# Kernel tuning notes

Measured on AMD Instinct MI355X. Metric: run time of the kernel, lower is better.

## Reference

```python
import jax, jax.numpy as jnp
import numpy as np

TEMPERATURE = 0.07
BASE_TEMPERATURE = 0.07
ANCHOR_NUM = 256   # total_classes after hard-anchor sampling
N_VIEW = 16
FEAT_DIM = 256
NUM_CLASSES = 19


def setup_inputs() -> dict:
    key = jax.random.key(0)
    k1, k2 = jax.random.split(key)
    feats = jax.random.normal(k1, (ANCHOR_NUM, N_VIEW, FEAT_DIM), dtype=jnp.float32)
    # projection-head outputs are L2-normalized in the upstream network
    feats = feats / jnp.linalg.norm(feats, axis=-1, keepdims=True)
    labels = jax.random.randint(k2, (ANCHOR_NUM,), 0, NUM_CLASSES, dtype=jnp.int32)
    return {"feats": feats, "labels": labels}


def reference(feats, labels) -> jnp.ndarray:
    # feats: [A, V, D] sampled anchors; labels: [A] class ids
    A, V, D = feats.shape
    N = A * V
    dt = feats.dtype
    # torch.cat(torch.unbind(feats_, dim=1), dim=0) -> view-major ordering
    contrast = feats.transpose(1, 0, 2).reshape(N, D)          # [N, D]
    lbl = jnp.tile(labels, V)                                   # [N]

    logits = jnp.matmul(contrast, contrast.T) / jnp.asarray(TEMPERATURE, dt)  # [N, N]
    logits = logits - jax.lax.stop_gradient(jnp.max(logits, axis=1, keepdims=True))

    pos_mask = (lbl[:, None] == lbl[None, :]).astype(dt)        # [N, N]
    neg_mask = 1.0 - pos_mask
    diag = jnp.arange(N)
    pos_mask = pos_mask.at[diag, diag].set(0.0)                 # drop self-contrast

    exp_logits = jnp.exp(logits)
    neg_sum = jnp.sum(exp_logits * neg_mask, axis=1, keepdims=True)  # [N, 1]
    log_prob = logits - jnp.log(exp_logits + neg_sum)
    mean_log_prob_pos = jnp.sum(pos_mask * log_prob, axis=1) / jnp.sum(pos_mask, axis=1)
    loss = -(TEMPERATURE / BASE_TEMPERATURE) * mean_log_prob_pos
    return jnp.mean(loss)
```

## Files before the change

### kernel.cpp

```cpp
#include <hip/hip_runtime.h>
#include <hip/hip_bf16.h>

#define D_DIM   256
#define N_TOT   4096
#define N_ANCH  256
#define NGRP    32
#define NBLK    528
#define NPART   64
#define K1  20.60992915555662f
#define LN2 0.6931471805599453f
#define MAXNP    48

typedef __attribute__((ext_vector_type(8))) short bf16x8;
typedef __attribute__((ext_vector_type(4))) float f32x4;

#define MFMA(a, b, c) __builtin_amdgcn_mfma_f32_16x16x32_bf16((a), (b), (c), 0, 0, 0)

__device__ __forceinline__ bf16x8 cvt8(const float4 a, const float4 b) {
    union { uint32_t w[4]; bf16x8 v; } u;
    asm("v_cvt_pk_bf16_f32 %0, %1, %2" : "=v"(u.w[0]) : "v"(a.x), "v"(a.y));
    asm("v_cvt_pk_bf16_f32 %0, %1, %2" : "=v"(u.w[1]) : "v"(a.z), "v"(a.w));
    asm("v_cvt_pk_bf16_f32 %0, %1, %2" : "=v"(u.w[2]) : "v"(b.x), "v"(b.y));
    asm("v_cvt_pk_bf16_f32 %0, %1, %2" : "=v"(u.w[3]) : "v"(b.z), "v"(b.w));
    return u.v;
}

__global__ void __launch_bounds__(256, 2) k_pass1(const float* __restrict__ feats,
                                                  const int* __restrict__ labels,
                                                  float* __restrict__ partAll,
                                                  float* __restrict__ posBuf,
                                                  float* __restrict__ out) {
    __shared__ __align__(16) char lds[65536];
    __shared__ int labS[N_ANCH];
    __shared__ int cntS[32];
    __shared__ int metaRank[16], metaToff[16];

    if (blockIdx.x == 0 && threadIdx.x == 0) out[0] = 0.f;

    int swzId = (blockIdx.x & 7) * 66 + (blockIdx.x >> 3);
    int rem = swzId, g = 0;
    while (rem >= NGRP - g) { rem -= NGRP - g; ++g; }
    const int s = g + rem;

    const int tid = threadIdx.x;
    const int lane = tid & 63, wid = tid >> 6;
    const int lrow = lane & 15, khalf = lane >> 4;
    const int wr = wid >> 1, wc = wid & 1;

    labS[tid] = labels[tid];
    if (tid < 32) cntS[tid] = 0;
    __syncthreads();
    atomicAdd(&cntS[labS[tid]], 1);

    const char* aSrcF = (const char*)(feats + (size_t)g * 128 * D_DIM);
    const char* bSrcF = (const char*)(feats + (size_t)s * 128 * D_DIM);

    uint32_t LgF[8], Lw[8];
#pragma unroll
    for (int o = 0; o < 8; ++o) {
        uint32_t L = (uint32_t)(tid * 16 + o * 4096);
        LgF[o] = (L >> 8) * 1024 + ((L & 255) << 1);
        Lw[o]  = L ^ (((L >> 8) & 7u) << 4);
    }

    auto stage = [&](int kc) {
        float4 fa[8][2], fb[8][2];
#pragma unroll
        for (int o = 0; o < 8; ++o) {
            const char* pa = aSrcF + LgF[o] + kc * 512;
            const char* pb = bSrcF + LgF[o] + kc * 512;
            fa[o][0] = *(const float4*)pa;  fa[o][1] = *(const float4*)(pa + 16);
            fb[o][0] = *(const float4*)pb;  fb[o][1] = *(const float4*)(pb + 16);
        }
#pragma unroll
        for (int o = 0; o < 8; ++o) {
            *(bf16x8*)(lds + Lw[o])         = cvt8(fa[o][0], fa[o][1]);
            *(bf16x8*)(lds + 32768 + Lw[o]) = cvt8(fb[o][0], fb[o][1]);
        }
    };

    f32x4 acc[4][4];
#pragma unroll
    for (int m = 0; m < 4; ++m)
#pragma unroll
        for (int n = 0; n < 4; ++n)
            acc[m][n] = (f32x4){0.f, 0.f, 0.f, 0.f};

    const uint32_t swz = (uint32_t)((lrow & 7) << 4);
    auto compute = [&]() {
#pragma unroll
        for (int ks = 0; ks < 4; ++ks) {
            bf16x8 af[4], bfr[4];
#pragma unroll
            for (int m = 0; m < 4; ++m) {
                uint32_t row = (uint32_t)(wr * 64 + m * 16 + lrow);
                af[m] = *(const bf16x8*)(lds + ((row * 256 + ks * 64 + khalf * 16) ^ swz));
            }
#pragma unroll
            for (int n = 0; n < 4; ++n) {
                uint32_t row = (uint32_t)(wc * 64 + n * 16 + lrow);
                bfr[n] = *(const bf16x8*)(lds + 32768 + ((row * 256 + ks * 64 + khalf * 16) ^ swz));
            }
#pragma unroll
            for (int m = 0; m < 4; ++m)
#pragma unroll
                for (int n = 0; n < 4; ++n)
                    acc[m][n] = MFMA(af[m], bfr[n], acc[m][n]);
        }
    };

    stage(0);
    __syncthreads();

    {
        int aIdx = tid >> 4, q = tid & 15;
        int aAnchor = (aIdx < 8) ? (g * 8 + aIdx) : (s * 8 + aIdx - 8);
        int la = labS[aAnchor];
        int rk = 0, tf = 0;
        for (int b = q; b < aAnchor; b += 16) {
            int lb = labS[b];
            rk += (lb == la);
            tf += cntS[lb];
        }
#pragma unroll
        for (int msk = 1; msk < 16; msk <<= 1) {
            rk += __shfl_xor(rk, msk, 64);
            tf += __shfl_xor(tf, msk, 64);
        }
        if (q == 0) { metaRank[aIdx] = rk; metaToff[aIdx] = tf; }
    }

    compute();
    __syncthreads();
    stage(1);
    __syncthreads();
    compute();
    __syncthreads();

    const int raBase = g * 8 + wr * 4, caBase = s * 8 + wc * 4;
    int labR[4], offR[4], rankR[4], labC[4], rankC[4], offC[4];
#pragma unroll
    for (int m = 0; m < 4; ++m) {
        labR[m]  = labS[raBase + m];
        offR[m]  = metaToff[wr * 4 + m];
        rankR[m] = metaRank[wr * 4 + m];
    }
#pragma unroll
    for (int n = 0; n < 4; ++n) {
        labC[n]  = labS[caBase + n];
        rankC[n] = metaRank[8 + wc * 4 + n];
        offC[n]  = metaToff[8 + wc * 4 + n];
    }

    float aAll[4][4];
    float colP[4];
#pragma unroll
    for (int m = 0; m < 4; ++m)
#pragma unroll
        for (int i = 0; i < 4; ++i) aAll[m][i] = 0.f;
#pragma unroll
    for (int n = 0; n < 4; ++n) colP[n] = 0.f;

    float* scr = (float*)lds + wid * 256;

#pragma unroll
    for (int m = 0; m < 4; ++m) {
#pragma unroll
        for (int n = 0; n < 4; ++n) {
            f32x4 c = acc[m][n];
            float e[4];
#pragma unroll
            for (int i = 0; i < 4; ++i) {
                e[i] = exp2f(__builtin_fmaf(c[i], K1, -K1));
                aAll[m][i] += e[i];
            }
            if (g != s)
                colP[n] += e[0] + e[1] + e[2] + e[3];
            if (labR[m] == labC[n]) {
                *(f32x4*)(posBuf + (size_t)(offR[m] + rankC[n]) * 256 + lane * 4) = c;
                if (g != s) {
#pragma unroll
                    for (int i = 0; i < 4; ++i)
                        scr[(khalf * 4 + i) * 16 + lrow] = c[i];
                    __builtin_amdgcn_s_waitcnt(0);
                    f32x4 tr = *(f32x4*)(scr + lrow * 16 + khalf * 4);
                    *(f32x4*)(posBuf + (size_t)(offC[n] + rankR[m]) * 256 + lane * 4) = tr;
                }
            }
        }
    }

#pragma unroll
    for (int msk = 1; msk < 16; msk <<= 1)
#pragma unroll
        for (int m = 0; m < 4; ++m)
#pragma unroll
            for (int i = 0; i < 4; ++i)
                aAll[m][i] += __shfl_xor(aAll[m][i], msk, 64);

    if (lrow == 0) {
#pragma unroll
        for (int m = 0; m < 4; ++m)
#pragma unroll
            for (int i = 0; i < 4; ++i) {
                int row = g * 128 + wr * 64 + m * 16 + khalf * 4 + i;
                partAll[row * NPART + s * 2 + wc] = aAll[m][i];
            }
    }

    if (g != s) {
#pragma unroll
        for (int msk = 16; msk < 64; msk <<= 1)
#pragma unroll
            for (int n = 0; n < 4; ++n)
                colP[n] += __shfl_xor(colP[n], msk, 64);
        if (lane < 16) {
#pragma unroll
            for (int n = 0; n < 4; ++n) {
                int row = s * 128 + wc * 64 + n * 16 + lane;
                partAll[row * NPART + g * 2 + wr] = colP[n];
            }
        }
    }
}

__global__ void __launch_bounds__(256) k_passB(const float* __restrict__ posBuf,
                                               const int* __restrict__ labels,
                                               const float* __restrict__ partAll,
                                               float* __restrict__ out) {
    int rt  = blockIdx.x;
    int tid = threadIdx.x;
    int l = tid >> 2, i = tid & 3;
    int r   = (l >> 4) * 4 + i;
    int col = l & 15;

    __shared__ float tile[MAXNP * 256];
    __shared__ float shA[16][17];
    __shared__ float shB[16][17];
    __shared__ float nsSh[16], PSh[16];
    __shared__ int labS[N_ANCH];
    __shared__ int cntS[32];
    __shared__ int wRk[4], wTf[4];
    __shared__ int mNp, mOff, mRank;

    labS[tid] = labels[tid];
    if (tid < 32) cntS[tid] = 0;
    __syncthreads();
    atomicAdd(&cntS[labS[tid]], 1);
    __syncthreads();
    {
        int la = labS[rt];
        int rk = 0, tf = 0;
        if (tid < rt) { int lb = labS[tid]; rk = (lb == la) ? 1 : 0; tf = cntS[lb]; }
#pragma unroll
        for (int msk = 1; msk < 64; msk <<= 1) {
            rk += __shfl_xor(rk, msk, 64);
            tf += __shfl_xor(tf, msk, 64);
        }
        if ((tid & 63) == 0) { wRk[tid >> 6] = rk; wTf[tid >> 6] = tf; }
        __syncthreads();
        if (tid == 0) {
            mNp   = cntS[la];
            mRank = wRk[0] + wRk[1] + wRk[2] + wRk[3];
            mOff  = wTf[0] + wTf[1] + wTf[2] + wTf[3];
        }
        __syncthreads();
    }
    int np = mNp, off = mOff, selfRank = mRank;

    float sE = 0.f, sP = 0.f;
    const float* src = posBuf + (size_t)off * 256 + tid;
    for (int j = 0; j < np; ++j) {
        float c = src[j * 256];
        tile[j * 256 + tid] = c;
        float l2 = __builtin_fmaf(c, K1, -K1);
        sE += exp2f(l2);
        bool diag = (j == selfRank) & (col == r);
        sP += diag ? 0.f : l2;
    }
    shA[r][col] = sE;
    shB[r][col] = sP;
    __syncthreads();
    if (tid < 16) {
        float e = 0.f, p = 0.f;
#pragma unroll
        for (int cc = 0; cc < 16; ++cc) { e += shA[tid][cc]; p += shB[tid][cc]; }
        const float* pa = partAll + (size_t)(rt * 16 + tid) * NPART;
        float sall = 0.f;
#pragma unroll
        for (int q = 0; q < 16; ++q) {
            float4 v = *(const float4*)(pa + q * 4);
            sall += v.x + v.y + v.z + v.w;
        }
        nsSh[tid] = sall - e;
        PSh[tid]  = p;
    }
    __syncthreads();

    float nsv = nsSh[r];
    float sL = 0.f;
    for (int j = 0; j < np; ++j) {
        float c  = tile[j * 256 + tid];
        float l2 = __builtin_fmaf(c, K1, -K1);
        float lg = __log2f(exp2f(l2) + nsv);
        bool diag = (j == selfRank) & (col == r);
        sL += diag ? 0.f : lg;
    }
    __syncthreads();
    shA[r][col] = sL;
    __syncthreads();
    if (tid < 16) {
        float L = 0.f;
#pragma unroll
        for (int cc = 0; cc < 16; ++cc) L += shA[tid][cc];
        float npRow = (float)(16 * np - 1);
        shB[0][tid] = (PSh[tid] - L) / npRow;
    }
    __syncthreads();
    if (tid == 0) {
        float sx = 0.f;
#pragma unroll
        for (int q = 0; q < 16; ++q) sx += shB[0][q];
        atomicAdd(out, -sx * (LN2 / (float)N_TOT));
    }
}

extern "C" void kernel_launch(void* const* d_in, const int* in_sizes, int n_in,
                              void* d_out, int out_size, void* d_ws, size_t ws_size,
                              hipStream_t stream) {
    const float* feats  = (const float*)d_in[0];
    const int*   labels = (const int*)d_in[1];
    float* out = (float*)d_out;

    char* ws = (char*)d_ws;
    float*  partAll = (float*)(ws + (2u << 20));
    float*  posBuf  = (float*)(ws + (3u << 20));

    k_pass1<<<NBLK, 256, 0, stream>>>(feats, labels, partAll, posBuf, out);
    k_passB<<<N_ANCH, 256, 0, stream>>>(posBuf, labels, partAll, out);
}
```

Before: 32.55 us.

## Pair diagonal tiles per block and load shared operand once for diagonal tiles

Splits the upper-triangular tile grid into 496 off-diagonal blocks plus 16 blocks that each process two diagonal tiles, reducing the grid from 528 to 512 blocks so it fits whole waves. Diagonal tiles now stage only the A operand and reuse it as B, halving their global loads and conversions. The second K-chunk of A is prefetched into registers before the first compute. This raises register pressure, and the diagonal-tile blocks run two tiles in sequence, which can lengthen the tail.

```diff
diff --git a/kernel.cpp b/kernel.cpp
--- a/kernel.cpp
+++ b/kernel.cpp
@@ -5,7 +5,8 @@
 #define N_TOT   4096
 #define N_ANCH  256
 #define NGRP    32
-#define NBLK    528
+#define NOFF    496
+#define NBLK    512
 #define NPART   64
 #define K1  20.60992915555662f
 #define LN2 0.6931471805599453f
@@ -37,11 +38,6 @@
 
     if (blockIdx.x == 0 && threadIdx.x == 0) out[0] = 0.f;
 
-    int swzId = (blockIdx.x & 7) * 66 + (blockIdx.x >> 3);
-    int rem = swzId, g = 0;
-    while (rem >= NGRP - g) { rem -= NGRP - g; ++g; }
-    const int s = g + rem;
-
     const int tid = threadIdx.x;
     const int lane = tid & 63, wid = tid >> 6;
     const int lrow = lane & 15, khalf = lane >> 4;
@@ -52,9 +48,6 @@
     __syncthreads();
     atomicAdd(&cntS[labS[tid]], 1);
 
-    const char* aSrcF = (const char*)(feats + (size_t)g * 128 * D_DIM);
-    const char* bSrcF = (const char*)(feats + (size_t)s * 128 * D_DIM);
-
     uint32_t LgF[8], Lw[8];
 #pragma unroll
     for (int o = 0; o < 8; ++o) {
@@ -62,165 +55,211 @@
         LgF[o] = (L >> 8) * 1024 + ((L & 255) << 1);
         Lw[o]  = L ^ (((L >> 8) & 7u) << 4);
     }
-
-    auto stage = [&](int kc) {
-        float4 fa[8][2], fb[8][2];
+    const uint32_t swz = (uint32_t)((lrow & 7) << 4);
+
+    auto gemm_tile = [&](int g, int s) {
+        const bool diag = (g == s);
+        const char* aSrcF = (const char*)(feats + (size_t)g * 128 * D_DIM);
+        const char* bSrcF = (const char*)(feats + (size_t)s * 128 * D_DIM);
+        const uint32_t bBase = diag ? 0u : 32768u;
+
+        f32x4 acc[4][4];
+#pragma unroll
+        for (int m = 0; m < 4; ++m)
+#pragma unroll
+            for (int n = 0; n < 4; ++n)
+                acc[m][n] = (f32x4){0.f, 0.f, 0.f, 0.f};
+
+        auto compute = [&]() {
+#pragma unroll
+            for (int ks = 0; ks < 4; ++ks) {
+                bf16x8 af[4], bfr[4];
+#pragma unroll
+                for (int m = 0; m < 4; ++m) {
+                    uint32_t row = (uint32_t)(wr * 64 + m * 16 + lrow);
+                    af[m] = *(const bf16x8*)(lds + ((row * 256 + ks * 64 + khalf * 16) ^ swz));
+                }
+#pragma unroll
+                for (int n = 0; n < 4; ++n) {
+                    uint32_t row = (uint32_t)(wc * 64 + n * 16 + lrow);
+                    bfr[n] = *(const bf16x8*)(lds + bBase + ((row * 256 + ks * 64 + khalf * 16) ^ swz));
+                }
+#pragma unroll
+                for (int m = 0; m < 4; ++m)
+#pragma unroll
+                    for (int n = 0; n < 4; ++n)
+                        acc[m][n] = MFMA(af[m], bfr[n], acc[m][n]);
+            }
+        };
+
+        {
+            float4 fa[8][2], fb[8][2];
+#pragma unroll
+            for (int o = 0; o < 8; ++o) {
+                const char* pa = aSrcF + LgF[o];
+                fa[o][0] = *(const float4*)pa;  fa[o][1] = *(const float4*)(pa + 16);
+            }
+            if (!diag) {
+#pragma unroll
+                for (int o = 0; o < 8; ++o) {
+                    const char* pb = bSrcF + LgF[o];
+                    fb[o][0] = *(const float4*)pb;  fb[o][1] = *(const float4*)(pb + 16);
+                }
+            }
+#pragma unroll
+            for (int o = 0; o < 8; ++o)
+                *(bf16x8*)(lds + Lw[o]) = cvt8(fa[o][0], fa[o][1]);
+            if (!diag) {
+#pragma unroll
+                for (int o = 0; o < 8; ++o)
+                    *(bf16x8*)(lds + 32768 + Lw[o]) = cvt8(fb[o][0], fb[o][1]);
+            }
+        }
+        __syncthreads();
+
+        float4 pfa[8][2];
 #pragma unroll
         for (int o = 0; o < 8; ++o) {
-            const char* pa = aSrcF + LgF[o] + kc * 512;
-            const char* pb = bSrcF + LgF[o] + kc * 512;
-            fa[o][0] = *(const float4*)pa;  fa[o][1] = *(const float4*)(pa + 16);
-            fb[o][0] = *(const float4*)pb;  fb[o][1] = *(const float4*)(pb + 16);
-        }
-#pragma unroll
-        for (int o = 0; o < 8; ++o) {
-            *(bf16x8*)(lds + Lw[o])         = cvt8(fa[o][0], fa[o][1]);
-            *(bf16x8*)(lds + 32768 + Lw[o]) = cvt8(fb[o][0], fb[o][1]);
-        }
+            const char* pa = aSrcF + LgF[o] + 512;
+            pfa[o][0] = *(const float4*)pa;  pfa[o][1] = *(const float4*)(pa + 16);
+        }
+
+        {
+            int aIdx = tid >> 4, q = tid & 15;
+            int aAnchor = (aIdx < 8) ? (g * 8 + aIdx) : (s * 8 + aIdx - 8);
+            int la = labS[aAnchor];
+            int rk = 0, tf = 0;
+            for (int b = q; b < aAnchor; b += 16) {
+                int lb = labS[b];
+                rk += (lb == la);
+                tf += cntS[lb];
+            }
+#pragma unroll
+            for (int msk = 1; msk < 16; msk <<= 1) {
+                rk += __shfl_xor(rk, msk, 64);
+                tf += __shfl_xor(tf, msk, 64);
+            }
+            if (q == 0) { metaRank[aIdx] = rk; metaToff[aIdx] = tf; }
+        }
+
+        compute();
+        __syncthreads();
+
+#pragma unroll
+        for (int o = 0; o < 8; ++o)
+            *(bf16x8*)(lds + Lw[o]) = cvt8(pfa[o][0], pfa[o][1]);
+        if (!diag) {
+            float4 fb[8][2];
+#pragma unroll
+            for (int o = 0; o < 8; ++o) {
+                const char* pb = bSrcF + LgF[o] + 512;
+                fb[o][0] = *(const float4*)pb;  fb[o][1] = *(const float4*)(pb + 16);
+            }
+#pragma unroll
+            for (int o = 0; o < 8; ++o)
+                *(bf16x8*)(lds + 32768 + Lw[o]) = cvt8(fb[o][0], fb[o][1]);
+        }
+        __syncthreads();
+        compute();
+        __syncthreads();
+
+        const int raBase = g * 8 + wr * 4, caBase = s * 8 + wc * 4;
+        int labR[4], offR[4], rankR[4], labC[4], rankC[4], offC[4];
+#pragma unroll
+        for (int m = 0; m < 4; ++m) {
+            labR[m]  = labS[raBase + m];
+            offR[m]  = metaToff[wr * 4 + m];
+            rankR[m] = metaRank[wr * 4 + m];
+        }
+#pragma unroll
+        for (int n = 0; n < 4; ++n) {
+            labC[n]  = labS[caBase + n];
+            rankC[n] = metaRank[8 + wc * 4 + n];
+            offC[n]  = metaToff[8 + wc * 4 + n];
+        }
+
+        float aAll[4][4];
+        float colP[4];
+#pragma unroll
+        for (int m = 0; m < 4; ++m)
+#pragma unroll
+            for (int i = 0; i < 4; ++i) aAll[m][i] = 0.f;
+#pragma unroll
+        for (int n = 0; n < 4; ++n) colP[n] = 0.f;
+
+        float* scr = (float*)lds + wid * 256;
+
+#pragma unroll
+        for (int m = 0; m < 4; ++m) {
+#pragma unroll
+            for (int n = 0; n < 4; ++n) {
+                f32x4 c = acc[m][n];
+                float e[4];
+#pragma unroll
+                for (int i = 0; i < 4; ++i) {
+                    e[i] = exp2f(__builtin_fmaf(c[i], K1, -K1));
+                    aAll[m][i] += e[i];
+                }
+                if (!diag)
+                    colP[n] += e[0] + e[1] + e[2] + e[3];
+                if (labR[m] == labC[n]) {
+                    *(f32x4*)(posBuf + (size_t)(offR[m] + rankC[n]) * 256 + lane * 4) = c;
+                    if (!diag) {
+#pragma unroll
+                        for (int i = 0; i < 4; ++i)
+                            scr[(khalf * 4 + i) * 16 + lrow] = c[i];
+                        __builtin_amdgcn_s_waitcnt(0);
+                        f32x4 tr = *(f32x4*)(scr + lrow * 16 + khalf * 4);
+                        *(f32x4*)(posBuf + (size_t)(offC[n] + rankR[m]) * 256 + lane * 4) = tr;
+                    }
+                }
+            }
+        }
+
+#pragma unroll
+        for (int msk = 1; msk < 16; msk <<= 1)
+#pragma unroll
+            for (int m = 0; m < 4; ++m)
+#pragma unroll
+                for (int i = 0; i < 4; ++i)
+                    aAll[m][i] += __shfl_xor(aAll[m][i], msk, 64);
+
+        if (lrow == 0) {
+#pragma unroll
+            for (int m = 0; m < 4; ++m)
+#pragma unroll
+                for (int i = 0; i < 4; ++i) {
+                    int row = g * 128 + wr * 64 + m * 16 + khalf * 4 + i;
+                    partAll[row * NPART + s * 2 + wc] = aAll[m][i];
+                }
+        }
+
+        if (!diag) {
+#pragma unroll
+            for (int msk = 16; msk < 64; msk <<= 1)
+#pragma unroll
+                for (int n = 0; n < 4; ++n)
+                    colP[n] += __shfl_xor(colP[n], msk, 64);
+            if (lane < 16) {
+#pragma unroll
+                for (int n = 0; n < 4; ++n) {
+                    int row = s * 128 + wc * 64 + n * 16 + lane;
+                    partAll[row * NPART + g * 2 + wr] = colP[n];
+                }
+            }
+        }
+        __syncthreads();
     };
 
-    f32x4 acc[4][4];
-#pragma unroll
-    for (int m = 0; m < 4; ++m)
-#pragma unroll
-        for (int n = 0; n < 4; ++n)
-            acc[m][n] = (f32x4){0.f, 0.f, 0.f, 0.f};
-
-    const uint32_t swz = (uint32_t)((lrow & 7) << 4);
-    auto compute = [&]() {
-#pragma unroll
-        for (int ks = 0; ks < 4; ++ks) {
-            bf16x8 af[4], bfr[4];
-#pragma unroll
-            for (int m = 0; m < 4; ++m) {
-                uint32_t row = (uint32_t)(wr * 64 + m * 16 + lrow);
-                af[m] = *(const bf16x8*)(lds + ((row * 256 + ks * 64 + khalf * 16) ^ swz));
-            }
-#pragma unroll
-            for (int n = 0; n < 4; ++n) {
-                uint32_t row = (uint32_t)(wc * 64 + n * 16 + lrow);
-                bfr[n] = *(const bf16x8*)(lds + 32768 + ((row * 256 + ks * 64 + khalf * 16) ^ swz));
-            }
-#pragma unroll
-            for (int m = 0; m < 4; ++m)
-#pragma unroll
-                for (int n = 0; n < 4; ++n)
-                    acc[m][n] = MFMA(af[m], bfr[n], acc[m][n]);
-        }
-    };
-
-    stage(0);
-    __syncthreads();
-
-    {
-        int aIdx = tid >> 4, q = tid & 15;
-        int aAnchor = (aIdx < 8) ? (g * 8 + aIdx) : (s * 8 + aIdx - 8);
-        int la = labS[aAnchor];
-        int rk = 0, tf = 0;
-        for (int b = q; b < aAnchor; b += 16) {
-            int lb = labS[b];
-            rk += (lb == la);
-            tf += cntS[lb];
-        }
-#pragma unroll
-        for (int msk = 1; msk < 16; msk <<= 1) {
-            rk += __shfl_xor(rk, msk, 64);
-            tf += __shfl_xor(tf, msk, 64);
-        }
-        if (q == 0) { metaRank[aIdx] = rk; metaToff[aIdx] = tf; }
-    }
-
-    compute();
-    __syncthreads();
-    stage(1);
-    __syncthreads();
-    compute();
-    __syncthreads();
-
-    const int raBase = g * 8 + wr * 4, caBase = s * 8 + wc * 4;
-    int labR[4], offR[4], rankR[4], labC[4], rankC[4], offC[4];
-#pragma unroll
-    for (int m = 0; m < 4; ++m) {
-        labR[m]  = labS[raBase + m];
-        offR[m]  = metaToff[wr * 4 + m];
-        rankR[m] = metaRank[wr * 4 + m];
-    }
-#pragma unroll
-    for (int n = 0; n < 4; ++n) {
-        labC[n]  = labS[caBase + n];
-        rankC[n] = metaRank[8 + wc * 4 + n];
-        offC[n]  = metaToff[8 + wc * 4 + n];
-    }
-
-    float aAll[4][4];
-    float colP[4];
-#pragma unroll
-    for (int m = 0; m < 4; ++m)
-#pragma unroll
-        for (int i = 0; i < 4; ++i) aAll[m][i] = 0.f;
-#pragma unroll
-    for (int n = 0; n < 4; ++n) colP[n] = 0.f;
-
-    float* scr = (float*)lds + wid * 256;
-
-#pragma unroll
-    for (int m = 0; m < 4; ++m) {
-#pragma unroll
-        for (int n = 0; n < 4; ++n) {
-            f32x4 c = acc[m][n];
-            float e[4];
-#pragma unroll
-            for (int i = 0; i < 4; ++i) {
-                e[i] = exp2f(__builtin_fmaf(c[i], K1, -K1));
-                aAll[m][i] += e[i];
-            }
-            if (g != s)
-                colP[n] += e[0] + e[1] + e[2] + e[3];
-            if (labR[m] == labC[n]) {
-                *(f32x4*)(posBuf + (size_t)(offR[m] + rankC[n]) * 256 + lane * 4) = c;
-                if (g != s) {
-#pragma unroll
-                    for (int i = 0; i < 4; ++i)
-                        scr[(khalf * 4 + i) * 16 + lrow] = c[i];
-                    __builtin_amdgcn_s_waitcnt(0);
-                    f32x4 tr = *(f32x4*)(scr + lrow * 16 + khalf * 4);
-                    *(f32x4*)(posBuf + (size_t)(offC[n] + rankR[m]) * 256 + lane * 4) = tr;
-                }
-            }
-        }
-    }
-
-#pragma unroll
-    for (int msk = 1; msk < 16; msk <<= 1)
-#pragma unroll
-        for (int m = 0; m < 4; ++m)
-#pragma unroll
-            for (int i = 0; i < 4; ++i)
-                aAll[m][i] += __shfl_xor(aAll[m][i], msk, 64);
-
-    if (lrow == 0) {
-#pragma unroll
-        for (int m = 0; m < 4; ++m)
-#pragma unroll
-            for (int i = 0; i < 4; ++i) {
-                int row = g * 128 + wr * 64 + m * 16 + khalf * 4 + i;
-                partAll[row * NPART + s * 2 + wc] = aAll[m][i];
-            }
-    }
-
-    if (g != s) {
-#pragma unroll
-        for (int msk = 16; msk < 64; msk <<= 1)
-#pragma unroll
-            for (int n = 0; n < 4; ++n)
-                colP[n] += __shfl_xor(colP[n], msk, 64);
-        if (lane < 16) {
-#pragma unroll
-            for (int n = 0; n < 4; ++n) {
-                int row = s * 128 + wc * 64 + n * 16 + lane;
-                partAll[row * NPART + g * 2 + wr] = colP[n];
-            }
-        }
+    if (blockIdx.x < NOFF) {
+        int swzId = (blockIdx.x & 7) * 62 + (blockIdx.x >> 3);
+        int rem = swzId, g = 0;
+        while (rem >= NGRP - 1 - g) { rem -= NGRP - 1 - g; ++g; }
+        gemm_tile(g, g + 1 + rem);
+    } else {
+        int j = blockIdx.x - NOFF;
+        gemm_tile(2 * j, 2 * j);
+        gemm_tile(2 * j + 1, 2 * j + 1);
     }
 }
 
```

After: 30.87 us. -5.2%, faster.
